# Performance work log

Hardware: AMD Instinct MI355X
Metric: run time of the kernel (lower is better)

The kernel has to match this reference:

```python
import jax, jax.numpy as jnp
import numpy as np
from jax import lax

S = 9      # patch feature size (3x3 flattened)
HID = 15   # MI-net hidden width
B = 4096
IMG = 192
PAD = 6


def _linear_params(k, fin, fout):
    bound = 1.0 / np.sqrt(fin)
    kw, kb = jax.random.split(k)
    w = jax.random.uniform(kw, (fout, fin), minval=-bound, maxval=bound, dtype=jnp.float32)
    b = jax.random.uniform(kb, (fout,), minval=-bound, maxval=bound, dtype=jnp.float32)
    return w, b


def setup_inputs() -> dict:
    key = jax.random.key(0)
    ks = jax.random.split(key, 12)
    x = jax.random.normal(ks[0], (B, 1, IMG, IMG), dtype=jnp.float32)
    hc = IMG // 3  # conv output side (stride-3 valid conv)
    ij = jax.random.randint(ks[1], (B, 2), 0, hc, dtype=jnp.int32)
    perm = jax.random.permutation(ks[2], B).astype(jnp.int32)
    cb = 1.0 / np.sqrt(1 * 3 * 3)
    conv_w = jax.random.uniform(ks[3], (1, 1, 3, 3), minval=-cb, maxval=cb, dtype=jnp.float32)
    conv_b = jax.random.uniform(ks[4], (1,), minval=-cb, maxval=cb, dtype=jnp.float32)
    xw1, xb1 = _linear_params(ks[5], S, S)
    xw2, xb2 = _linear_params(ks[6], S, S)
    xw3, xb3 = _linear_params(ks[7], S, HID)
    yw1, yb1 = _linear_params(ks[8], S, S)
    yw2, yb2 = _linear_params(ks[9], S, S)
    yw3, yb3 = _linear_params(ks[10], S, HID)
    fw, fb = _linear_params(ks[11], HID, 1)
    return dict(x=x, ij=ij, perm=perm, conv_w=conv_w, conv_b=conv_b,
                xw1=xw1, xb1=xb1, xw2=xw2, xb2=xb2, xw3=xw3, xb3=xb3,
                yw1=yw1, yb1=yb1, yw2=yw2, yb2=yb2, yw3=yw3, yb3=yb3,
                fw=fw, fb=fb)


def _mi_net(p1, p2, xw1, xb1, xw2, xb2, xw3, xb3,
            yw1, yb1, yw2, yb2, yw3, yb3, fw, fb):
    ix = p1 + jax.nn.relu(p1 @ xw1.T + xb1)
    ix = ix + jax.nn.relu(ix @ xw2.T + xb2)
    ix = ix @ xw3.T + xb3
    iy = p2 + jax.nn.relu(p2 @ yw1.T + yb1)
    iy = iy + jax.nn.relu(iy @ yw2.T + yb2)
    iy = iy @ yw3.T + yb3
    h1 = jax.nn.relu(ix + iy)
    return h1 @ fw.T + fb  # [B, 1]


def reference(x, ij, perm, conv_w, conv_b,
              xw1, xb1, xw2, xb2, xw3, xb3,
              yw1, yb1, yw2, yb2, yw3, yb3, fw, fb):
    # stride-3 valid conv: [B,1,IMG,IMG] -> [B,1,64,64]
    co = lax.conv_general_dilated(x, conv_w, (3, 3), 'VALID',
                                  dimension_numbers=('NCHW', 'OIHW', 'NCHW'))
    co = co[:, 0] + conv_b[0]  # [B, Hc, Wc]
    bn, hc, wc = co.shape
    # pad_circular(data, 6)[i:i+3, j:j+6] == data[(i-6+r) % Hc, (j-6+c) % Wc]
    rows = (ij[:, 0:1] - PAD + jnp.arange(3, dtype=jnp.int32)) % hc  # [B,3]
    cols = (ij[:, 1:2] - PAD + jnp.arange(6, dtype=jnp.int32)) % wc  # [B,6]
    rect = co[jnp.arange(bn)[:, None, None], rows[:, :, None], cols[:, None, :]]  # [B,3,6]
    patch1 = rect[:, :, :3].reshape(-1, S)
    patch2 = rect[:, :, 3:].reshape(-1, S)
    patch2_sh = patch2[perm]
    pred_xy = _mi_net(patch1, patch2, xw1, xb1, xw2, xb2, xw3, xb3,
                      yw1, yb1, yw2, yb2, yw3, yb3, fw, fb)
    pred_x_y = _mi_net(patch1, patch2_sh, xw1, xb1, xw2, xb2, xw3, xb3,
                       yw1, yb1, yw2, yb2, yw3, yb3, fw, fb)
    ret = jnp.mean(pred_xy) - jnp.log(jnp.mean(jnp.exp(pred_x_y)))
    return -ret
```

## Files before the change

### kernel.cpp

```cpp
#include <hip/hip_runtime.h>
#include <math.h>

#define BATCH 4096
#define IMGD 192
#define HC 64
#define PADV 6
#define NBLK2 256
#define IPB 16

#define XB 0
#define YB 432
#define W1O 0
#define W2O 108
#define W3O 216
#define B1O 396
#define B2O 405
#define B3O 414
#define FWO 864
#define FBO 879

__global__ __launch_bounds__(256) void k_fused(
    const float* __restrict__ x, const int* __restrict__ ij,
    const int* __restrict__ perm,
    const float* __restrict__ cw, const float* __restrict__ cb,
    const float* __restrict__ xw1, const float* __restrict__ xb1,
    const float* __restrict__ xw2, const float* __restrict__ xb2,
    const float* __restrict__ xw3, const float* __restrict__ xb3,
    const float* __restrict__ yw1, const float* __restrict__ yb1,
    const float* __restrict__ yw2, const float* __restrict__ yb2,
    const float* __restrict__ yw3, const float* __restrict__ yb3,
    const float* __restrict__ fw, const float* __restrict__ fb,
    float* __restrict__ partials)
{
    __shared__ __align__(16) float s[880];
    __shared__ __align__(16) int   ija[BATCH * 2];
    __shared__ int   pidx[IPB];
    __shared__ float lpatch[IPB * 27];
    __shared__ float bout[48 * 15];

    int t  = threadIdx.x;
    int b0 = blockIdx.x * IPB;

    {
        int4* d = (int4*)ija;
        const int4* g = (const int4*)ij;
        #pragma unroll
        for (int i = 0; i < 8; ++i) d[t + 256 * i] = g[t + 256 * i];
    }
    if (t < IPB) pidx[t] = perm[b0 + t];

    for (int i = t; i < 108; i += 256) {
        int row = i / 12, col = i - row * 12;
        if (col < 9) {
            int src = row * 9 + col;
            s[XB + W1O + i] = xw1[src];  s[XB + W2O + i] = xw2[src];
            s[YB + W1O + i] = yw1[src];  s[YB + W2O + i] = yw2[src];
        }
    }
    for (int i = t; i < 180; i += 256) {
        int row = i / 12, col = i - row * 12;
        if (col < 9) {
            int src = row * 9 + col;
            s[XB + W3O + i] = xw3[src];  s[YB + W3O + i] = yw3[src];
        }
    }
    if (t >= 192) {
        int tb = t - 192;
        if (tb < 9)       { s[XB + B1O + tb] = xb1[tb];  s[XB + B2O + tb] = xb2[tb];
                            s[YB + B1O + tb] = yb1[tb];  s[YB + B2O + tb] = yb2[tb]; }
        else if (tb < 24) { int j = tb - 9;  s[XB + B3O + j] = xb3[j];  s[YB + B3O + j] = yb3[j]; }
        else if (tb < 39) { int j = tb - 24; s[FWO + j] = fw[j]; }
        else if (tb == 39){ s[FBO] = fb[0]; }
    }

    float w[9];
    #pragma unroll
    for (int i = 0; i < 9; ++i) w[i] = cw[i];
    float cbias = cb[0];
    __syncthreads();

    {
        int idxA = t;
        int itemA = idxA / 27;  int pA = idxA - itemA * 27;
        int rA, cA, selA, slotA;
        if (pA < 18) { rA = pA / 6; cA = pA - rA * 6; selA = 0;
                       int h = (cA >= 3); slotA = h * 9 + rA * 3 + (cA - 3 * h); }
        else         { int q = pA - 18; rA = q / 3; cA = 3 + q - rA * 3; selA = 1; slotA = 18 + q; }
        int bbA = selA ? pidx[itemA] : (b0 + itemA);
        int i0A = ija[2 * bbA], j0A = ija[2 * bbA + 1];
        int rrA = i0A - PADV + rA;  if (rrA < 0) rrA += HC;
        int ccA = j0A - PADV + cA;  if (ccA < 0) ccA += HC;
        const float* pa = x + (size_t)bbA * (IMGD * IMGD) + (size_t)(rrA * 3) * IMGD + ccA * 3;

        bool hasB = (t < 176);
        int idxB = t + 256;
        int itemB = idxB / 27;  int pB = idxB - itemB * 27;
        int rB, cB, selB, slotB;
        if (pB < 18) { rB = pB / 6; cB = pB - rB * 6; selB = 0;
                       int h = (cB >= 3); slotB = h * 9 + rB * 3 + (cB - 3 * h); }
        else         { int q = pB - 18; rB = q / 3; cB = 3 + q - rB * 3; selB = 1; slotB = 18 + q; }
        itemB = hasB ? itemB : 0;
        int bbB = selB ? pidx[itemB] : (b0 + itemB);
        int i0B = ija[2 * bbB], j0B = ija[2 * bbB + 1];
        int rrB = i0B - PADV + rB;  if (rrB < 0) rrB += HC;
        int ccB = j0B - PADV + cB;  if (ccB < 0) ccB += HC;
        const float* pb = hasB ? (x + (size_t)bbB * (IMGD * IMGD) + (size_t)(rrB * 3) * IMGD + ccB * 3)
                               : pa;

        float a0 = pa[0],          a1 = pa[1],            a2 = pa[2];
        float a3 = pa[IMGD],       a4 = pa[IMGD + 1],     a5 = pa[IMGD + 2];
        float a6 = pa[2 * IMGD],   a7 = pa[2 * IMGD + 1], a8 = pa[2 * IMGD + 2];
        float e0 = pb[0],          e1 = pb[1],            e2 = pb[2];
        float e3 = pb[IMGD],       e4 = pb[IMGD + 1],     e5 = pb[IMGD + 2];
        float e6 = pb[2 * IMGD],   e7 = pb[2 * IMGD + 1], e8 = pb[2 * IMGD + 2];

        float vA = cbias + a0*w[0] + a1*w[1] + a2*w[2] + a3*w[3] + a4*w[4]
                         + a5*w[5] + a6*w[6] + a7*w[7] + a8*w[8];
        lpatch[itemA * 27 + slotA] = vA;
        if (hasB) {
            float vB = cbias + e0*w[0] + e1*w[1] + e2*w[2] + e3*w[3] + e4*w[4]
                             + e5*w[5] + e6*w[6] + e7*w[7] + e8*w[8];
            lpatch[itemB * 27 + slotB] = vB;
        }
    }
    __syncthreads();

    {
        int wv = t >> 6, l = t & 63;
        if (wv < 3 && l < 16) {
            int woff = (wv == 0) ? XB : YB;
            int ib = wv * 16 + l;
            float p[9];
            #pragma unroll
            for (int k = 0; k < 9; ++k) p[k] = lpatch[l * 27 + wv * 9 + k];

            float v[9];
            #pragma unroll
            for (int j = 0; j < 9; ++j) {
                const float4 r0 = *(const float4*)&s[woff + W1O + j * 12];
                const float4 r1 = *(const float4*)&s[woff + W1O + j * 12 + 4];
                float acc = s[woff + B1O + j]
                    + r0.x*p[0] + r0.y*p[1] + r0.z*p[2] + r0.w*p[3]
                    + r1.x*p[4] + r1.y*p[5] + r1.z*p[6] + r1.w*p[7]
                    + s[woff + W1O + j * 12 + 8] * p[8];
                v[j] = p[j] + fmaxf(acc, 0.0f);
            }
            float u[9];
            #pragma unroll
            for (int j = 0; j < 9; ++j) {
                const float4 r0 = *(const float4*)&s[woff + W2O + j * 12];
                const float4 r1 = *(const float4*)&s[woff + W2O + j * 12 + 4];
                float acc = s[woff + B2O + j]
                    + r0.x*v[0] + r0.y*v[1] + r0.z*v[2] + r0.w*v[3]
                    + r1.x*v[4] + r1.y*v[5] + r1.z*v[6] + r1.w*v[7]
                    + s[woff + W2O + j * 12 + 8] * v[8];
                u[j] = v[j] + fmaxf(acc, 0.0f);
            }
            #pragma unroll
            for (int j = 0; j < 15; ++j) {
                const float4 r0 = *(const float4*)&s[woff + W3O + j * 12];
                const float4 r1 = *(const float4*)&s[woff + W3O + j * 12 + 4];
                float acc = s[woff + B3O + j]
                    + r0.x*u[0] + r0.y*u[1] + r0.z*u[2] + r0.w*u[3]
                    + r1.x*u[4] + r1.y*u[5] + r1.z*u[6] + r1.w*u[7]
                    + s[woff + W3O + j * 12 + 8] * u[8];
                bout[ib * 15 + j] = acc;
            }
        }
    }
    __syncthreads();

    if (t < IPB) {
        float fbv = s[FBO];
        float pxy = fbv, pxs = fbv;
        #pragma unroll
        for (int j = 0; j < 15; ++j) {
            float oxj  = bout[t * 15 + j];
            float oyj  = bout[(16 + t) * 15 + j];
            float oysj = bout[(32 + t) * 15 + j];
            float fwj  = s[FWO + j];
            pxy += fmaxf(oxj + oyj,  0.0f) * fwj;
            pxs += fmaxf(oxj + oysj, 0.0f) * fwj;
        }
        float e = expf(pxs);
        #pragma unroll
        for (int o = 8; o > 0; o >>= 1) {
            pxy += __shfl_down(pxy, o);
            e   += __shfl_down(e, o);
        }
        if (t == 0) {
            partials[blockIdx.x]         = pxy;
            partials[NBLK2 + blockIdx.x] = e;
        }
    }
}

__global__ __launch_bounds__(256) void k_final(const float* __restrict__ partials,
                                               float* __restrict__ out)
{
    __shared__ float r1[4], r2[4];
    int t = threadIdx.x;
    float sx = partials[t];
    float se = partials[NBLK2 + t];
    #pragma unroll
    for (int o = 32; o > 0; o >>= 1) {
        sx += __shfl_down(sx, o);
        se += __shfl_down(se, o);
    }
    int wid = t >> 6, lane = t & 63;
    if (lane == 0) { r1[wid] = sx; r2[wid] = se; }
    __syncthreads();
    if (t == 0) {
        float S = (r1[0] + r1[1]) + (r1[2] + r1[3]);
        float E = (r2[0] + r2[1]) + (r2[2] + r2[3]);
        out[0] = logf(E / (float)BATCH) - S / (float)BATCH;
    }
}

extern "C" void kernel_launch(void* const* d_in, const int* in_sizes, int n_in,
                              void* d_out, int out_size, void* d_ws, size_t ws_size,
                              hipStream_t stream)
{
    const float* x    = (const float*)d_in[0];
    const int*   ij   = (const int*)d_in[1];
    const int*   perm = (const int*)d_in[2];
    const float* cw   = (const float*)d_in[3];
    const float* cb   = (const float*)d_in[4];
    const float* xw1  = (const float*)d_in[5];
    const float* xb1  = (const float*)d_in[6];
    const float* xw2  = (const float*)d_in[7];
    const float* xb2  = (const float*)d_in[8];
    const float* xw3  = (const float*)d_in[9];
    const float* xb3  = (const float*)d_in[10];
    const float* yw1  = (const float*)d_in[11];
    const float* yb1  = (const float*)d_in[12];
    const float* yw2  = (const float*)d_in[13];
    const float* yb2  = (const float*)d_in[14];
    const float* yw3  = (const float*)d_in[15];
    const float* yb3  = (const float*)d_in[16];
    const float* fw   = (const float*)d_in[17];
    const float* fb   = (const float*)d_in[18];

    float* partials = (float*)d_ws;

    k_fused<<<NBLK2, 256, 0, stream>>>(x, ij, perm, cw, cb,
                                       xw1, xb1, xw2, xb2, xw3, xb3,
                                       yw1, yb1, yw2, yb2, yw3, yb3,
                                       fw, fb, partials);
    k_final<<<1, 256, 0, stream>>>(partials, (float*)d_out);
}
```

Measured before the change: 12.73 us.

## Fuse final reduction via last-block atomic counter and drop full ij staging

Replaces the separate final-reduction kernel with a last-block-done pattern: each block bumps a global atomic counter, and the last one sums the partials and writes the output. It stops copying the whole ij array (32 KB) into shared memory per block and gathers only the needed index pairs. It also halves items per block and doubles the grid to 512 blocks. This removes one kernel launch and large shared-memory traffic, at the cost of an extra memset launch, atomics and fences.

```diff
diff --git a/kernel.cpp b/kernel.cpp
--- a/kernel.cpp
+++ b/kernel.cpp
@@ -5,8 +5,8 @@
 #define IMGD 192
 #define HC 64
 #define PADV 6
-#define NBLK2 256
-#define IPB 16
+#define NBLK 512
+#define IPB 8
 
 #define XB 0
 #define YB 432
@@ -19,7 +19,7 @@
 #define FWO 864
 #define FBO 879
 
-__global__ __launch_bounds__(256) void k_fused(
+__global__ __launch_bounds__(256) void k_all(
     const float* __restrict__ x, const int* __restrict__ ij,
     const int* __restrict__ perm,
     const float* __restrict__ cw, const float* __restrict__ cb,
@@ -30,23 +30,20 @@
     const float* __restrict__ yw2, const float* __restrict__ yb2,
     const float* __restrict__ yw3, const float* __restrict__ yb3,
     const float* __restrict__ fw, const float* __restrict__ fb,
-    float* __restrict__ partials)
+    float* __restrict__ partials,
+    int* __restrict__ counter,
+    float* __restrict__ out)
 {
     __shared__ __align__(16) float s[880];
-    __shared__ __align__(16) int   ija[BATCH * 2];
     __shared__ int   pidx[IPB];
+    __shared__ int   ij4[IPB * 4];
     __shared__ float lpatch[IPB * 27];
-    __shared__ float bout[48 * 15];
+    __shared__ float bout[3 * IPB * 15];
+    __shared__ int   amlast;
 
     int t  = threadIdx.x;
     int b0 = blockIdx.x * IPB;
 
-    {
-        int4* d = (int4*)ija;
-        const int4* g = (const int4*)ij;
-        #pragma unroll
-        for (int i = 0; i < 8; ++i) d[t + 256 * i] = g[t + 256 * i];
-    }
     if (t < IPB) pidx[t] = perm[b0 + t];
 
     for (int i = t; i < 108; i += 256) {
@@ -77,59 +74,43 @@
     #pragma unroll
     for (int i = 0; i < 9; ++i) w[i] = cw[i];
     float cbias = cb[0];
-    __syncthreads();
-
-    {
-        int idxA = t;
-        int itemA = idxA / 27;  int pA = idxA - itemA * 27;
-        int rA, cA, selA, slotA;
-        if (pA < 18) { rA = pA / 6; cA = pA - rA * 6; selA = 0;
-                       int h = (cA >= 3); slotA = h * 9 + rA * 3 + (cA - 3 * h); }
-        else         { int q = pA - 18; rA = q / 3; cA = 3 + q - rA * 3; selA = 1; slotA = 18 + q; }
-        int bbA = selA ? pidx[itemA] : (b0 + itemA);
-        int i0A = ija[2 * bbA], j0A = ija[2 * bbA + 1];
-        int rrA = i0A - PADV + rA;  if (rrA < 0) rrA += HC;
-        int ccA = j0A - PADV + cA;  if (ccA < 0) ccA += HC;
-        const float* pa = x + (size_t)bbA * (IMGD * IMGD) + (size_t)(rrA * 3) * IMGD + ccA * 3;
-
-        bool hasB = (t < 176);
-        int idxB = t + 256;
-        int itemB = idxB / 27;  int pB = idxB - itemB * 27;
-        int rB, cB, selB, slotB;
-        if (pB < 18) { rB = pB / 6; cB = pB - rB * 6; selB = 0;
-                       int h = (cB >= 3); slotB = h * 9 + rB * 3 + (cB - 3 * h); }
-        else         { int q = pB - 18; rB = q / 3; cB = 3 + q - rB * 3; selB = 1; slotB = 18 + q; }
-        itemB = hasB ? itemB : 0;
-        int bbB = selB ? pidx[itemB] : (b0 + itemB);
-        int i0B = ija[2 * bbB], j0B = ija[2 * bbB + 1];
-        int rrB = i0B - PADV + rB;  if (rrB < 0) rrB += HC;
-        int ccB = j0B - PADV + cB;  if (ccB < 0) ccB += HC;
-        const float* pb = hasB ? (x + (size_t)bbB * (IMGD * IMGD) + (size_t)(rrB * 3) * IMGD + ccB * 3)
-                               : pa;
-
-        float a0 = pa[0],          a1 = pa[1],            a2 = pa[2];
-        float a3 = pa[IMGD],       a4 = pa[IMGD + 1],     a5 = pa[IMGD + 2];
-        float a6 = pa[2 * IMGD],   a7 = pa[2 * IMGD + 1], a8 = pa[2 * IMGD + 2];
-        float e0 = pb[0],          e1 = pb[1],            e2 = pb[2];
-        float e3 = pb[IMGD],       e4 = pb[IMGD + 1],     e5 = pb[IMGD + 2];
-        float e6 = pb[2 * IMGD],   e7 = pb[2 * IMGD + 1], e8 = pb[2 * IMGD + 2];
-
-        float vA = cbias + a0*w[0] + a1*w[1] + a2*w[2] + a3*w[3] + a4*w[4]
-                         + a5*w[5] + a6*w[6] + a7*w[7] + a8*w[8];
-        lpatch[itemA * 27 + slotA] = vA;
-        if (hasB) {
-            float vB = cbias + e0*w[0] + e1*w[1] + e2*w[2] + e3*w[3] + e4*w[4]
-                             + e5*w[5] + e6*w[6] + e7*w[7] + e8*w[8];
-            lpatch[itemB * 27 + slotB] = vB;
-        }
+
+    __syncthreads();
+    if (t < 2 * IPB) {
+        int item = t & (IPB - 1);
+        int sel  = t >> 3;
+        int bb   = sel ? pidx[item] : (b0 + item);
+        ij4[item * 4 + sel * 2 + 0] = ij[2 * bb];
+        ij4[item * 4 + sel * 2 + 1] = ij[2 * bb + 1];
+    }
+    __syncthreads();
+
+    if (t < IPB * 27) {
+        int item = t / 27;  int p = t - item * 27;
+        int r, c, sel, slot;
+        if (p < 18) { r = p / 6; c = p - r * 6; sel = 0;
+                      int h = (c >= 3); slot = h * 9 + r * 3 + (c - 3 * h); }
+        else        { int q = p - 18; r = q / 3; c = 3 + q - r * 3; sel = 1; slot = 18 + q; }
+        int bb = sel ? pidx[item] : (b0 + item);
+        int i0 = ij4[item * 4 + sel * 2], j0 = ij4[item * 4 + sel * 2 + 1];
+        int rr = i0 - PADV + r;  if (rr < 0) rr += HC;
+        int cc = j0 - PADV + c;  if (cc < 0) cc += HC;
+        const float* xp = x + (size_t)bb * (IMGD * IMGD)
+                            + (size_t)(rr * 3) * IMGD + cc * 3;
+        float a0 = xp[0],        a1 = xp[1],            a2 = xp[2];
+        float a3 = xp[IMGD],     a4 = xp[IMGD + 1],     a5 = xp[IMGD + 2];
+        float a6 = xp[2*IMGD],   a7 = xp[2*IMGD + 1],   a8 = xp[2*IMGD + 2];
+        float v = cbias + a0*w[0] + a1*w[1] + a2*w[2] + a3*w[3] + a4*w[4]
+                        + a5*w[5] + a6*w[6] + a7*w[7] + a8*w[8];
+        lpatch[item * 27 + slot] = v;
     }
     __syncthreads();
 
     {
         int wv = t >> 6, l = t & 63;
-        if (wv < 3 && l < 16) {
+        if (wv < 3 && l < IPB) {
             int woff = (wv == 0) ? XB : YB;
-            int ib = wv * 16 + l;
+            int ib = wv * IPB + l;
             float p[9];
             #pragma unroll
             for (int k = 0; k < 9; ++k) p[k] = lpatch[l * 27 + wv * 9 + k];
@@ -176,44 +157,43 @@
         #pragma unroll
         for (int j = 0; j < 15; ++j) {
             float oxj  = bout[t * 15 + j];
-            float oyj  = bout[(16 + t) * 15 + j];
-            float oysj = bout[(32 + t) * 15 + j];
+            float oyj  = bout[(IPB + t) * 15 + j];
+            float oysj = bout[(2 * IPB + t) * 15 + j];
             float fwj  = s[FWO + j];
             pxy += fmaxf(oxj + oyj,  0.0f) * fwj;
             pxs += fmaxf(oxj + oysj, 0.0f) * fwj;
         }
         float e = expf(pxs);
         #pragma unroll
-        for (int o = 8; o > 0; o >>= 1) {
+        for (int o = IPB / 2; o > 0; o >>= 1) {
             pxy += __shfl_down(pxy, o);
             e   += __shfl_down(e, o);
         }
         if (t == 0) {
-            partials[blockIdx.x]         = pxy;
-            partials[NBLK2 + blockIdx.x] = e;
-        }
-    }
-}
-
-__global__ __launch_bounds__(256) void k_final(const float* __restrict__ partials,
-                                               float* __restrict__ out)
-{
-    __shared__ float r1[4], r2[4];
-    int t = threadIdx.x;
-    float sx = partials[t];
-    float se = partials[NBLK2 + t];
-    #pragma unroll
-    for (int o = 32; o > 0; o >>= 1) {
-        sx += __shfl_down(sx, o);
-        se += __shfl_down(se, o);
-    }
-    int wid = t >> 6, lane = t & 63;
-    if (lane == 0) { r1[wid] = sx; r2[wid] = se; }
-    __syncthreads();
+            partials[blockIdx.x]        = pxy;
+            partials[NBLK + blockIdx.x] = e;
+        }
+    }
+
     if (t == 0) {
-        float S = (r1[0] + r1[1]) + (r1[2] + r1[3]);
-        float E = (r2[0] + r2[1]) + (r2[2] + r2[3]);
-        out[0] = logf(E / (float)BATCH) - S / (float)BATCH;
+        __threadfence();
+        int old = atomicAdd(counter, 1);
+        amlast = (old == NBLK - 1);
+    }
+    __syncthreads();
+    if (amlast && t < 64) {
+        __threadfence();
+        float sx = 0.0f, se = 0.0f;
+        #pragma unroll
+        for (int k = 0; k < NBLK / 64; ++k) sx += partials[t + 64 * k];
+        #pragma unroll
+        for (int k = 0; k < NBLK / 64; ++k) se += partials[NBLK + t + 64 * k];
+        #pragma unroll
+        for (int o = 32; o > 0; o >>= 1) {
+            sx += __shfl_down(sx, o);
+            se += __shfl_down(se, o);
+        }
+        if (t == 0) out[0] = logf(se / (float)BATCH) - sx / (float)BATCH;
     }
 }
 
@@ -242,10 +222,12 @@
     const float* fb   = (const float*)d_in[18];
 
     float* partials = (float*)d_ws;
-
-    k_fused<<<NBLK2, 256, 0, stream>>>(x, ij, perm, cw, cb,
-                                       xw1, xb1, xw2, xb2, xw3, xb3,
-                                       yw1, yb1, yw2, yb2, yw3, yb3,
-                                       fw, fb, partials);
-    k_final<<<1, 256, 0, stream>>>(partials, (float*)d_out);
+    int*   counter  = (int*)((float*)d_ws + 2 * NBLK);
+
+    hipMemsetAsync((void*)counter, 0, 4, stream);
+
+    k_all<<<NBLK, 256, 0, stream>>>(x, ij, perm, cw, cb,
+                                    xw1, xb1, xw2, xb2, xw3, xb3,
+                                    yw1, yb1, yw2, yb2, yw3, yb3,
+                                    fw, fb, partials, counter, (float*)d_out);
 }
```

Measured after the change: 25.82 us. 103% more time.
